# Kernel optimization log

Hardware: AMD Instinct MI355X
Metric: run time of the kernel (lower is better)

The kernel has to match this reference:

```python
import jax, jax.numpy as jnp
import numpy as np

H_IMG, W_IMG = 32, 32   # image_size -> seq_len = 1024
NH, HD, D = 8, 32, 256  # num_heads, head_dim, d_model
B = 8


def _relative_positions(h, w):
    # Swin-style relative position index table, [h*w, h*w] int32
    y = np.arange(h); x = np.arange(w)
    coords = np.stack(np.meshgrid(y, x, indexing='ij')).reshape(2, -1)  # [2, S]
    rel = coords[:, :, None] - coords[:, None, :]                      # [2, S, S]
    rel = rel.transpose(1, 2, 0).astype(np.int64)                      # [S, S, 2]
    rel[:, :, 0] += h - 1
    rel[:, :, 1] += w - 1
    rel[:, :, 0] *= 2 * w - 1
    return np.int32(rel.sum(-1))                                       # [S, S]

_POS = _relative_positions(H_IMG, W_IMG)


def setup_inputs() -> dict:
    key = jax.random.key(0)
    ks = jax.random.split(key, 8)
    S = H_IMG * W_IMG
    return {
        'inputs_q': jax.random.normal(ks[0], (B, S, D), jnp.float32),
        'inputs_kv': jax.random.normal(ks[1], (B, S, D), jnp.float32),
        'Wq': jax.random.normal(ks[2], (D, NH, HD), jnp.float32) / np.sqrt(D),
        'bq': jnp.zeros((NH, HD), jnp.float32),
        'Wk': jax.random.normal(ks[3], (D, NH, HD), jnp.float32) / np.sqrt(D),
        'bk': jnp.zeros((NH, HD), jnp.float32),
        'Wv': jax.random.normal(ks[4], (D, NH, HD), jnp.float32) / np.sqrt(D),
        'bv': jnp.zeros((NH, HD), jnp.float32),
        'rel_table': 0.02 * jax.random.normal(ks[5], ((2 * H_IMG - 1) * (2 * W_IMG - 1), NH), jnp.float32),
        'Wo': jax.random.normal(ks[6], (NH, HD, D), jnp.float32) / np.sqrt(NH * HD),
        'bo': jnp.zeros((D,), jnp.float32),
    }


def reference(inputs_q, inputs_kv, Wq, bq, Wk, bk, Wv, bv, rel_table, Wo, bo):
    pos = jnp.asarray(_POS)                                  # [S, S] int32 (constant)
    q = jnp.einsum('bsd,dhk->bshk', inputs_q, Wq) + bq       # [B, S, H, HD]
    k = jnp.einsum('bsd,dhk->bshk', inputs_kv, Wk) + bk
    v = jnp.einsum('bsd,dhk->bshk', inputs_kv, Wv) + bv
    q = q / jnp.sqrt(jnp.asarray(HD, q.dtype))
    attn = jnp.einsum('bqhd,bkhd->bhqk', q, k)               # [B, H, S, S]
    rel_bias = rel_table[pos]                                # [S, S, H]
    attn = attn + jnp.transpose(rel_bias, (2, 0, 1))[None]   # broadcast over batch
    attn = jax.nn.softmax(attn, axis=-1)
    x = jnp.einsum('bhqk,bkhd->bqhd', attn, v)               # [B, S, H, HD]
    return jnp.einsum('bqhd,hdf->bqf', x, Wo) + bo           # [B, S, D]
```

## Files before the change

kernel.cpp:

```cpp
#include <hip/hip_runtime.h>
#include <hip/hip_bf16.h>

#define B_SZ   8
#define S_LEN  1024
#define D_MOD  256
#define NHEADS 8
#define H_IMG  32
#define W_IMG  32
#define M_ROWS (B_SZ * S_LEN)
#define LOG2E  1.4426950408889634f
#define QSCALE_LOG2E 0.2550352766751165f

typedef _Float16 f16x8 __attribute__((ext_vector_type(8)));
typedef _Float16 f16x4 __attribute__((ext_vector_type(4)));
typedef float    f32x4 __attribute__((ext_vector_type(4)));

__global__ __launch_bounds__(256)
void wtrans_kernel(const float* __restrict__ Wq, const float* __restrict__ Wk,
                   const float* __restrict__ Wv, const float* __restrict__ Wo,
                   _Float16* __restrict__ wt) {
    const int mi = blockIdx.x >> 3;
    const int k0 = (blockIdx.x & 7) << 5;
    const float* W = (mi == 0) ? Wq : (mi == 1) ? Wk : (mi == 2) ? Wv : Wo;
    const int n = threadIdx.x;
    const float* src = W + (size_t)k0 * 256 + n;
    _Float16* dst = wt + (size_t)mi * 65536 + (size_t)n * 256 + k0;
#pragma unroll
    for (int g = 0; g < 4; ++g) {
        f16x8 o;
#pragma unroll
        for (int j = 0; j < 8; ++j) o[j] = (_Float16)src[(size_t)(g * 8 + j) * 256];
        *(f16x8*)(dst + g * 8) = o;
    }
}

__device__ inline void ldA16(const float* p, f16x8& x0, f16x8& x1) {
    f32x4 a = *(const f32x4*)p, b = *(const f32x4*)(p + 4);
    f32x4 c = *(const f32x4*)(p + 8), d = *(const f32x4*)(p + 12);
#pragma unroll
    for (int j = 0; j < 4; ++j) {
        x0[j] = (_Float16)a[j]; x0[4 + j] = (_Float16)b[j];
        x1[j] = (_Float16)c[j]; x1[4 + j] = (_Float16)d[j];
    }
}
__device__ inline void ldA16(const _Float16* p, f16x8& x0, f16x8& x1) {
    x0 = *(const f16x8*)p; x1 = *(const f16x8*)(p + 8);
}

template <typename InT, typename OutT, int VT_MODE>
__device__ inline void gemm_body(const InT* __restrict__ A, const _Float16* __restrict__ Wt,
                                 const float* __restrict__ bias, OutT* __restrict__ out,
                                 float scale, int m0, int n0) {
    __shared__ __align__(16) _Float16 As[2][64][72];
    __shared__ __align__(16) _Float16 Bt[2][64][72];
    const int tid  = threadIdx.x;
    const int w    = tid >> 6;
    const int lane = tid & 63;
    const int quad = lane >> 4;
    const int l16  = lane & 15;
    const int mq   = (w & 1) * 32;
    const int nq   = (w >> 1) * 32;

    const int srow = tid >> 2;
    const int scol = (tid & 3) << 4;
    const InT* Ap = A + (size_t)(m0 + srow) * 256 + scol;
    const _Float16* Bp = Wt + (size_t)(n0 + srow) * 256 + scol;

    f16x8 a0n, a1n, b0n, b1n;
    ldA16(Ap, a0n, a1n);
    b0n = *(const f16x8*)Bp; b1n = *(const f16x8*)(Bp + 8);
    *(f16x8*)(&As[0][srow][scol])     = a0n;
    *(f16x8*)(&As[0][srow][scol + 8]) = a1n;
    *(f16x8*)(&Bt[0][srow][scol])     = b0n;
    *(f16x8*)(&Bt[0][srow][scol + 8]) = b1n;
    __syncthreads();

    f32x4 acc[2][2];
#pragma unroll
    for (int i = 0; i < 2; ++i)
#pragma unroll
        for (int j = 0; j < 2; ++j) acc[i][j] = (f32x4){0.f, 0.f, 0.f, 0.f};

#pragma unroll
    for (int s = 0; s < 4; ++s) {
        const int cur = s & 1;
        if (s < 3) {
            ldA16(Ap + (s + 1) * 64, a0n, a1n);
            b0n = *(const f16x8*)(Bp + (s + 1) * 64);
            b1n = *(const f16x8*)(Bp + (s + 1) * 64 + 8);
        }
#pragma unroll
        for (int kk = 0; kk < 2; ++kk) {
            const int k8 = kk * 32 + quad * 8;
            f16x8 fa0 = *(const f16x8*)(&As[cur][mq + l16][k8]);
            f16x8 fa1 = *(const f16x8*)(&As[cur][mq + 16 + l16][k8]);
            f16x8 fb0 = *(const f16x8*)(&Bt[cur][nq + l16][k8]);
            f16x8 fb1 = *(const f16x8*)(&Bt[cur][nq + 16 + l16][k8]);
            acc[0][0] = __builtin_amdgcn_mfma_f32_16x16x32_f16(fa0, fb0, acc[0][0], 0, 0, 0);
            acc[0][1] = __builtin_amdgcn_mfma_f32_16x16x32_f16(fa0, fb1, acc[0][1], 0, 0, 0);
            acc[1][0] = __builtin_amdgcn_mfma_f32_16x16x32_f16(fa1, fb0, acc[1][0], 0, 0, 0);
            acc[1][1] = __builtin_amdgcn_mfma_f32_16x16x32_f16(fa1, fb1, acc[1][1], 0, 0, 0);
        }
        if (s < 3) {
            const int nxt = cur ^ 1;
            *(f16x8*)(&As[nxt][srow][scol])     = a0n;
            *(f16x8*)(&As[nxt][srow][scol + 8]) = a1n;
            *(f16x8*)(&Bt[nxt][srow][scol])     = b0n;
            *(f16x8*)(&Bt[nxt][srow][scol + 8]) = b1n;
            __syncthreads();
        }
    }

    if (VT_MODE) {
        const int b8 = (m0 >> 10) * 8;
#pragma unroll
        for (int nh = 0; nh < 2; ++nh) {
            const int col = n0 + nq + nh * 16 + l16;
            const float bv = bias[col];
#pragma unroll
            for (int mh = 0; mh < 2; ++mh) {
                const int row0 = (m0 & 1023) + mq + mh * 16 + quad * 4;
                f16x4 pk;
#pragma unroll
                for (int r = 0; r < 4; ++r) pk[r] = (_Float16)((acc[mh][nh][r] + bv) * scale);
                *(f16x4*)((_Float16*)out +
                          ((size_t)(b8 + (col >> 5)) * 32 + (col & 31)) * 1024 + row0) = pk;
            }
        }
    } else {
#pragma unroll
        for (int nh = 0; nh < 2; ++nh) {
            const int col = n0 + nq + nh * 16 + l16;
            const float bv = bias[col];
#pragma unroll
            for (int mh = 0; mh < 2; ++mh) {
#pragma unroll
                for (int r = 0; r < 4; ++r) {
                    const int row = m0 + mq + mh * 16 + quad * 4 + r;
                    out[(size_t)row * 256 + col] = (OutT)((acc[mh][nh][r] + bv) * scale);
                }
            }
        }
    }
}

__global__ __launch_bounds__(256)
void gemm_qkv_kernel(const float* __restrict__ in_q, const float* __restrict__ in_kv,
                     const _Float16* __restrict__ wt,
                     const float* __restrict__ bq, const float* __restrict__ bk,
                     const float* __restrict__ bv,
                     _Float16* __restrict__ qh, _Float16* __restrict__ kh,
                     _Float16* __restrict__ vt) {
    const int z = blockIdx.z;
    const int m0 = blockIdx.x * 64, n0 = blockIdx.y * 64;
    if (z == 0)
        gemm_body<float, _Float16, 0>(in_q, wt, bq, qh, QSCALE_LOG2E, m0, n0);
    else if (z == 1)
        gemm_body<float, _Float16, 0>(in_kv, wt + 65536, bk, kh, 1.0f, m0, n0);
    else
        gemm_body<float, _Float16, 1>(in_kv, wt + 2 * 65536, bv, vt, 1.0f, m0, n0);
}

__global__ __launch_bounds__(256)
void gemm_out_kernel(const _Float16* __restrict__ X, const _Float16* __restrict__ wt,
                     const float* __restrict__ bo, float* __restrict__ out) {
    gemm_body<_Float16, float, 0>(X, wt + (size_t)3 * 65536, bo, out, 1.0f,
                                  blockIdx.x * 64, blockIdx.y * 64);
}

__global__ __launch_bounds__(256)
void attn_kernel(const _Float16* __restrict__ q, const _Float16* __restrict__ k,
                 const _Float16* __restrict__ vt, const float* __restrict__ rel_table,
                 _Float16* __restrict__ xout) {
    __shared__ __align__(16) _Float16 Ps[4][2][32][40];
    __shared__ float bias_row[4][2][64];

    const int tid  = threadIdx.x;
    const int w    = tid >> 6;
    const int lane = tid & 63;
    const int quad = lane >> 4;
    const int l16  = lane & 15;

    const int n     = blockIdx.x;
    const int xcd   = n & 7;
    const int local = n >> 3;
    const int bh    = xcd * 8 + (local & 7);
    const int qc    = local >> 3;
    const int b     = bh >> 3, h = bh & 7;
    const int qrow_base = qc * 128 + w * 32;
    const int yq = qrow_base >> 5;

    const _Float16* qp = q + ((size_t)(b * S_LEN + qrow_base + l16)) * D_MOD + h * 32 + quad * 8;
    const f16x8 qf0 = *(const f16x8*)(qp);
    const f16x8 qf1 = *(const f16x8*)(qp + 16 * D_MOD);
    const _Float16* kp = k + ((size_t)(b * S_LEN + l16)) * D_MOD + h * 32 + quad * 8;
    const _Float16* vp = vt + ((size_t)(bh * 32 + l16)) * S_LEN + quad * 8;
    const float* bp = rel_table + ((size_t)(yq + 31) * 63 + lane) * NHEADS + h;

    f16x8 ones;
#pragma unroll
    for (int j = 0; j < 8; ++j) ones[j] = (_Float16)1.0f;

    f32x4 o00 = {0.f,0.f,0.f,0.f}, o01 = {0.f,0.f,0.f,0.f};
    f32x4 o10 = {0.f,0.f,0.f,0.f}, o11 = {0.f,0.f,0.f,0.f};
    f32x4 ol0 = {0.f,0.f,0.f,0.f}, ol1 = {0.f,0.f,0.f,0.f};

    if (lane < 63) bias_row[w][0][lane] = bp[0] * LOG2E;
    f16x8 kf0 = *(const f16x8*)(kp);
    f16x8 kf1 = *(const f16x8*)(kp + 16 * D_MOD);
    f16x8 vf0 = *(const f16x8*)(vp);
    f16x8 vf1 = *(const f16x8*)(vp + 16 * S_LEN);

    for (int kt = 0; kt < S_LEN / 32; ++kt) {
        const int cur = kt & 1, nxt = cur ^ 1;
        f16x8 nk0, nk1, nv0, nv1;
        float nb = 0.f;
        const bool more = (kt < S_LEN / 32 - 1);
        if (more) {
            const _Float16* kq = kp + (size_t)(kt + 1) * 32 * D_MOD;
            nk0 = *(const f16x8*)(kq);
            nk1 = *(const f16x8*)(kq + 16 * D_MOD);
            const _Float16* vq = vp + (kt + 1) * 32;
            nv0 = *(const f16x8*)(vq);
            nv1 = *(const f16x8*)(vq + 16 * S_LEN);
            if (lane < 63) nb = bp[-(ptrdiff_t)((kt + 1) * 63 * NHEADS)];
        }

#pragma unroll
        for (int mh = 0; mh < 2; ++mh) {
            const f16x8 qf = mh ? qf1 : qf0;
#pragma unroll
            for (int kh = 0; kh < 2; ++kh) {
                const int idx0 = mh * 16 + quad * 4 - kh * 16 - l16 + 31;
                const float* bb = &bias_row[w][cur][idx0];
                f32x4 c; c[0] = bb[0]; c[1] = bb[1]; c[2] = bb[2]; c[3] = bb[3];
                f32x4 s = __builtin_amdgcn_mfma_f32_16x16x32_f16(qf, kh ? kf1 : kf0, c, 0, 0, 0);
#pragma unroll
                for (int r = 0; r < 4; ++r)
                    Ps[w][cur][mh * 16 + quad * 4 + r][kh * 16 + l16] =
                        (_Float16)__builtin_amdgcn_exp2f(s[r]);
            }
        }

        const f16x8 pf0 = *(const f16x8*)(&Ps[w][cur][l16][quad * 8]);
        const f16x8 pf1 = *(const f16x8*)(&Ps[w][cur][16 + l16][quad * 8]);
        o00 = __builtin_amdgcn_mfma_f32_16x16x32_f16(pf0, vf0, o00, 0, 0, 0);
        o01 = __builtin_amdgcn_mfma_f32_16x16x32_f16(pf0, vf1, o01, 0, 0, 0);
        o10 = __builtin_amdgcn_mfma_f32_16x16x32_f16(pf1, vf0, o10, 0, 0, 0);
        o11 = __builtin_amdgcn_mfma_f32_16x16x32_f16(pf1, vf1, o11, 0, 0, 0);
        ol0 = __builtin_amdgcn_mfma_f32_16x16x32_f16(pf0, ones, ol0, 0, 0, 0);
        ol1 = __builtin_amdgcn_mfma_f32_16x16x32_f16(pf1, ones, ol1, 0, 0, 0);

        if (more) {
            if (lane < 63) bias_row[w][nxt][lane] = nb * LOG2E;
            kf0 = nk0; kf1 = nk1; vf0 = nv0; vf1 = nv1;
        }
    }

#pragma unroll
    for (int mh = 0; mh < 2; ++mh) {
        const f32x4 oa = mh ? o10 : o00;
        const f32x4 ob = mh ? o11 : o01;
        const f32x4 ll = mh ? ol1 : ol0;
#pragma unroll
        for (int r = 0; r < 4; ++r) {
            const float inv = __builtin_amdgcn_rcpf(ll[r]);
            const int qg = qrow_base + mh * 16 + quad * 4 + r;
            _Float16* op = xout + ((size_t)(b * S_LEN + qg)) * D_MOD + h * 32;
            op[l16]      = (_Float16)(oa[r] * inv);
            op[l16 + 16] = (_Float16)(ob[r] * inv);
        }
    }
}

extern "C" void kernel_launch(void* const* d_in, const int* in_sizes, int n_in,
                              void* d_out, int out_size, void* d_ws, size_t ws_size,
                              hipStream_t stream) {
    const float* in_q  = (const float*)d_in[0];
    const float* in_kv = (const float*)d_in[1];
    const float* Wq    = (const float*)d_in[2];
    const float* bq    = (const float*)d_in[3];
    const float* Wk    = (const float*)d_in[4];
    const float* bk    = (const float*)d_in[5];
    const float* Wv    = (const float*)d_in[6];
    const float* bv    = (const float*)d_in[7];
    const float* rel   = (const float*)d_in[8];
    const float* Wo    = (const float*)d_in[9];
    const float* bo    = (const float*)d_in[10];
    float* out = (float*)d_out;

    _Float16* qh = (_Float16*)d_ws;
    _Float16* kh = qh + (size_t)M_ROWS * D_MOD;
    _Float16* vt = kh + (size_t)M_ROWS * D_MOD;
    _Float16* xh = vt + (size_t)M_ROWS * D_MOD;
    _Float16* wt = xh + (size_t)M_ROWS * D_MOD;

    const dim3 blk(256);

    wtrans_kernel<<<dim3(32), blk, 0, stream>>>(Wq, Wk, Wv, Wo, wt);
    gemm_qkv_kernel<<<dim3(M_ROWS / 64, 4, 3), blk, 0, stream>>>(
        in_q, in_kv, wt, bq, bk, bv, qh, kh, vt);
    attn_kernel<<<dim3(512), blk, 0, stream>>>(qh, kh, vt, rel, xh);
    gemm_out_kernel<<<dim3(M_ROWS / 64, 4), blk, 0, stream>>>(xh, wt, bo, out);
}
```

Baseline: 142.9 us.

## Split attention keys across blocks, precompute bias table, fuse combine into output GEMM

Attention now splits the key range into two halves across twice as many blocks. Each block writes unnormalized fp32 partial outputs and row sums, and the output GEMM merges and normalizes them while loading its A operand. The relative-position bias is precomputed once into an MFMA-layout table in a merged prep kernel, which replaces the per-tile LDS staging, and the MFMA operands are swapped so P is written to LDS as vectorized stores. The GEMMs drop LDS double buffering for single buffers with an extra barrier and gain occupancy hints. The aim is more parallelism in attention and fewer LDS/bias ops, at the cost of extra fp32 partial traffic.

```diff
diff --git a/kernel.cpp b/kernel.cpp
--- a/kernel.cpp
+++ b/kernel.cpp
@@ -1,39 +1,19 @@
 #include <hip/hip_runtime.h>
-#include <hip/hip_bf16.h>
 
 #define B_SZ   8
 #define S_LEN  1024
 #define D_MOD  256
 #define NHEADS 8
-#define H_IMG  32
-#define W_IMG  32
 #define M_ROWS (B_SZ * S_LEN)
 #define LOG2E  1.4426950408889634f
 #define QSCALE_LOG2E 0.2550352766751165f
+#define NSPLIT 2
+#define TILES_PER_SPLIT 16
 
 typedef _Float16 f16x8 __attribute__((ext_vector_type(8)));
 typedef _Float16 f16x4 __attribute__((ext_vector_type(4)));
 typedef float    f32x4 __attribute__((ext_vector_type(4)));
 
-__global__ __launch_bounds__(256)
-void wtrans_kernel(const float* __restrict__ Wq, const float* __restrict__ Wk,
-                   const float* __restrict__ Wv, const float* __restrict__ Wo,
-                   _Float16* __restrict__ wt) {
-    const int mi = blockIdx.x >> 3;
-    const int k0 = (blockIdx.x & 7) << 5;
-    const float* W = (mi == 0) ? Wq : (mi == 1) ? Wk : (mi == 2) ? Wv : Wo;
-    const int n = threadIdx.x;
-    const float* src = W + (size_t)k0 * 256 + n;
-    _Float16* dst = wt + (size_t)mi * 65536 + (size_t)n * 256 + k0;
-#pragma unroll
-    for (int g = 0; g < 4; ++g) {
-        f16x8 o;
-#pragma unroll
-        for (int j = 0; j < 8; ++j) o[j] = (_Float16)src[(size_t)(g * 8 + j) * 256];
-        *(f16x8*)(dst + g * 8) = o;
-    }
-}
-
 __device__ inline void ldA16(const float* p, f16x8& x0, f16x8& x1) {
     f32x4 a = *(const f32x4*)p, b = *(const f32x4*)(p + 4);
     f32x4 c = *(const f32x4*)(p + 8), d = *(const f32x4*)(p + 12);
@@ -45,14 +25,52 @@
 }
 __device__ inline void ldA16(const _Float16* p, f16x8& x0, f16x8& x1) {
     x0 = *(const f16x8*)p; x1 = *(const f16x8*)(p + 8);
+}
+
+__global__ __launch_bounds__(256)
+void prep_kernel(const float* __restrict__ Wq, const float* __restrict__ Wk,
+                 const float* __restrict__ Wv, const float* __restrict__ Wo,
+                 const float* __restrict__ rel,
+                 _Float16* __restrict__ wt, float* __restrict__ tab) {
+    if (blockIdx.x < 32) {
+        const int mi = blockIdx.x >> 3;
+        const int k0 = (blockIdx.x & 7) << 5;
+        const float* W = (mi == 0) ? Wq : (mi == 1) ? Wk : (mi == 2) ? Wv : Wo;
+        const int n = threadIdx.x;
+        const float* src = W + (size_t)k0 * 256 + n;
+        _Float16* dst = wt + (size_t)mi * 65536 + (size_t)n * 256 + k0;
+#pragma unroll
+        for (int g = 0; g < 4; ++g) {
+            f16x8 o;
+#pragma unroll
+            for (int j = 0; j < 8; ++j) o[j] = (_Float16)src[(size_t)(g * 8 + j) * 256];
+            *(f16x8*)(dst + g * 8) = o;
+        }
+        return;
+    }
+    const int flat = (blockIdx.x - 32) * 256 + threadIdx.x;
+    const int lane = flat & 63;
+    const int t1   = flat >> 6;
+    const int e    = t1 % 3;
+    const int t2   = t1 / 3;
+    const int dy31 = t2 % 63;
+    const int h    = t2 / 63;
+    const int quad = lane >> 4, l16 = lane & 15;
+    f32x4 v;
+#pragma unroll
+    for (int reg = 0; reg < 4; ++reg) {
+        const int idx = 16 * e + l16 - quad * 4 - reg + 15;
+        v[reg] = rel[(size_t)(dy31 * 63 + idx) * NHEADS + h] * LOG2E;
+    }
+    *(f32x4*)(tab + (size_t)flat * 4) = v;
 }
 
 template <typename InT, typename OutT, int VT_MODE>
 __device__ inline void gemm_body(const InT* __restrict__ A, const _Float16* __restrict__ Wt,
                                  const float* __restrict__ bias, OutT* __restrict__ out,
                                  float scale, int m0, int n0) {
-    __shared__ __align__(16) _Float16 As[2][64][72];
-    __shared__ __align__(16) _Float16 Bt[2][64][72];
+    __shared__ __align__(16) _Float16 As[64][72];
+    __shared__ __align__(16) _Float16 Bt[64][72];
     const int tid  = threadIdx.x;
     const int w    = tid >> 6;
     const int lane = tid & 63;
@@ -69,11 +87,6 @@
     f16x8 a0n, a1n, b0n, b1n;
     ldA16(Ap, a0n, a1n);
     b0n = *(const f16x8*)Bp; b1n = *(const f16x8*)(Bp + 8);
-    *(f16x8*)(&As[0][srow][scol])     = a0n;
-    *(f16x8*)(&As[0][srow][scol + 8]) = a1n;
-    *(f16x8*)(&Bt[0][srow][scol])     = b0n;
-    *(f16x8*)(&Bt[0][srow][scol + 8]) = b1n;
-    __syncthreads();
 
     f32x4 acc[2][2];
 #pragma unroll
@@ -83,7 +96,12 @@
 
 #pragma unroll
     for (int s = 0; s < 4; ++s) {
-        const int cur = s & 1;
+        if (s) __syncthreads();
+        *(f16x8*)(&As[srow][scol])     = a0n;
+        *(f16x8*)(&As[srow][scol + 8]) = a1n;
+        *(f16x8*)(&Bt[srow][scol])     = b0n;
+        *(f16x8*)(&Bt[srow][scol + 8]) = b1n;
+        __syncthreads();
         if (s < 3) {
             ldA16(Ap + (s + 1) * 64, a0n, a1n);
             b0n = *(const f16x8*)(Bp + (s + 1) * 64);
@@ -92,22 +110,14 @@
 #pragma unroll
         for (int kk = 0; kk < 2; ++kk) {
             const int k8 = kk * 32 + quad * 8;
-            f16x8 fa0 = *(const f16x8*)(&As[cur][mq + l16][k8]);
-            f16x8 fa1 = *(const f16x8*)(&As[cur][mq + 16 + l16][k8]);
-            f16x8 fb0 = *(const f16x8*)(&Bt[cur][nq + l16][k8]);
-            f16x8 fb1 = *(const f16x8*)(&Bt[cur][nq + 16 + l16][k8]);
+            f16x8 fa0 = *(const f16x8*)(&As[mq + l16][k8]);
+            f16x8 fa1 = *(const f16x8*)(&As[mq + 16 + l16][k8]);
+            f16x8 fb0 = *(const f16x8*)(&Bt[nq + l16][k8]);
+            f16x8 fb1 = *(const f16x8*)(&Bt[nq + 16 + l16][k8]);
             acc[0][0] = __builtin_amdgcn_mfma_f32_16x16x32_f16(fa0, fb0, acc[0][0], 0, 0, 0);
             acc[0][1] = __builtin_amdgcn_mfma_f32_16x16x32_f16(fa0, fb1, acc[0][1], 0, 0, 0);
             acc[1][0] = __builtin_amdgcn_mfma_f32_16x16x32_f16(fa1, fb0, acc[1][0], 0, 0, 0);
             acc[1][1] = __builtin_amdgcn_mfma_f32_16x16x32_f16(fa1, fb1, acc[1][1], 0, 0, 0);
-        }
-        if (s < 3) {
-            const int nxt = cur ^ 1;
-            *(f16x8*)(&As[nxt][srow][scol])     = a0n;
-            *(f16x8*)(&As[nxt][srow][scol + 8]) = a1n;
-            *(f16x8*)(&Bt[nxt][srow][scol])     = b0n;
-            *(f16x8*)(&Bt[nxt][srow][scol + 8]) = b1n;
-            __syncthreads();
         }
     }
 
@@ -144,7 +154,7 @@
     }
 }
 
-__global__ __launch_bounds__(256)
+__global__ __launch_bounds__(256, 6)
 void gemm_qkv_kernel(const float* __restrict__ in_q, const float* __restrict__ in_kv,
                      const _Float16* __restrict__ wt,
                      const float* __restrict__ bq, const float* __restrict__ bk,
@@ -162,40 +172,127 @@
 }
 
 __global__ __launch_bounds__(256)
-void gemm_out_kernel(const _Float16* __restrict__ X, const _Float16* __restrict__ wt,
-                     const float* __restrict__ bo, float* __restrict__ out) {
-    gemm_body<_Float16, float, 0>(X, wt + (size_t)3 * 65536, bo, out, 1.0f,
-                                  blockIdx.x * 64, blockIdx.y * 64);
-}
-
-__global__ __launch_bounds__(256)
-void attn_kernel(const _Float16* __restrict__ q, const _Float16* __restrict__ k,
-                 const _Float16* __restrict__ vt, const float* __restrict__ rel_table,
-                 _Float16* __restrict__ xout) {
-    __shared__ __align__(16) _Float16 Ps[4][2][32][40];
-    __shared__ float bias_row[4][2][64];
-
+void gemm_out_kernel(const float* __restrict__ o0, const float* __restrict__ o1,
+                     const float* __restrict__ l0, const float* __restrict__ l1,
+                     const _Float16* __restrict__ wt4, const float* __restrict__ bo,
+                     float* __restrict__ out) {
+    __shared__ __align__(16) _Float16 As[64][72];
+    __shared__ __align__(16) _Float16 Bt[64][72];
     const int tid  = threadIdx.x;
     const int w    = tid >> 6;
     const int lane = tid & 63;
     const int quad = lane >> 4;
     const int l16  = lane & 15;
+    const int mq   = (w & 1) * 32;
+    const int nq   = (w >> 1) * 32;
+    const int m0   = blockIdx.x * 64, n0 = blockIdx.y * 64;
+
+    const int srow = tid >> 2;
+    const int scol = (tid & 3) << 4;
+    const size_t row = (size_t)(m0 + srow);
+    const _Float16* Bp = wt4 + (size_t)(n0 + srow) * 256 + scol;
+
+    f16x8 a0n, a1n, b0n, b1n;
+    auto ldX = [&](int s, f16x8& x0, f16x8& x1) {
+        const int col0 = s * 64 + scol;
+        const int head = col0 >> 5;
+        const float inv = __builtin_amdgcn_rcpf(l0[row * 8 + head] + l1[row * 8 + head]);
+        const float* p0 = o0 + row * 256 + col0;
+        const float* p1 = o1 + row * 256 + col0;
+        f32x4 u0 = *(const f32x4*)p0,       u1 = *(const f32x4*)(p0 + 4);
+        f32x4 u2 = *(const f32x4*)(p0 + 8), u3 = *(const f32x4*)(p0 + 12);
+        f32x4 v0 = *(const f32x4*)p1,       v1 = *(const f32x4*)(p1 + 4);
+        f32x4 v2 = *(const f32x4*)(p1 + 8), v3 = *(const f32x4*)(p1 + 12);
+#pragma unroll
+        for (int j = 0; j < 4; ++j) {
+            x0[j]     = (_Float16)((u0[j] + v0[j]) * inv);
+            x0[4 + j] = (_Float16)((u1[j] + v1[j]) * inv);
+            x1[j]     = (_Float16)((u2[j] + v2[j]) * inv);
+            x1[4 + j] = (_Float16)((u3[j] + v3[j]) * inv);
+        }
+    };
+
+    ldX(0, a0n, a1n);
+    b0n = *(const f16x8*)Bp; b1n = *(const f16x8*)(Bp + 8);
+
+    f32x4 acc[2][2];
+#pragma unroll
+    for (int i = 0; i < 2; ++i)
+#pragma unroll
+        for (int j = 0; j < 2; ++j) acc[i][j] = (f32x4){0.f, 0.f, 0.f, 0.f};
+
+#pragma unroll
+    for (int s = 0; s < 4; ++s) {
+        if (s) __syncthreads();
+        *(f16x8*)(&As[srow][scol])     = a0n;
+        *(f16x8*)(&As[srow][scol + 8]) = a1n;
+        *(f16x8*)(&Bt[srow][scol])     = b0n;
+        *(f16x8*)(&Bt[srow][scol + 8]) = b1n;
+        __syncthreads();
+        if (s < 3) {
+            ldX(s + 1, a0n, a1n);
+            b0n = *(const f16x8*)(Bp + (s + 1) * 64);
+            b1n = *(const f16x8*)(Bp + (s + 1) * 64 + 8);
+        }
+#pragma unroll
+        for (int kk = 0; kk < 2; ++kk) {
+            const int k8 = kk * 32 + quad * 8;
+            f16x8 fa0 = *(const f16x8*)(&As[mq + l16][k8]);
+            f16x8 fa1 = *(const f16x8*)(&As[mq + 16 + l16][k8]);
+            f16x8 fb0 = *(const f16x8*)(&Bt[nq + l16][k8]);
+            f16x8 fb1 = *(const f16x8*)(&Bt[nq + 16 + l16][k8]);
+            acc[0][0] = __builtin_amdgcn_mfma_f32_16x16x32_f16(fa0, fb0, acc[0][0], 0, 0, 0);
+            acc[0][1] = __builtin_amdgcn_mfma_f32_16x16x32_f16(fa0, fb1, acc[0][1], 0, 0, 0);
+            acc[1][0] = __builtin_amdgcn_mfma_f32_16x16x32_f16(fa1, fb0, acc[1][0], 0, 0, 0);
+            acc[1][1] = __builtin_amdgcn_mfma_f32_16x16x32_f16(fa1, fb1, acc[1][1], 0, 0, 0);
+        }
+    }
+
+#pragma unroll
+    for (int nh = 0; nh < 2; ++nh) {
+        const int col = n0 + nq + nh * 16 + l16;
+        const float bv = bo[col];
+#pragma unroll
+        for (int mh = 0; mh < 2; ++mh) {
+#pragma unroll
+            for (int r = 0; r < 4; ++r) {
+                const int rr = m0 + mq + mh * 16 + quad * 4 + r;
+                out[(size_t)rr * 256 + col] = (acc[mh][nh][r] + bv);
+            }
+        }
+    }
+}
+
+__global__ __launch_bounds__(256, 4)
+void attn_kernel(const _Float16* __restrict__ q, const _Float16* __restrict__ k,
+                 const _Float16* __restrict__ vt, const float* __restrict__ tab,
+                 float* __restrict__ opart, float* __restrict__ lpart) {
+    __shared__ __align__(16) _Float16 Ps[4][32][40];
+
+    const int tid  = threadIdx.x;
+    const int w    = tid >> 6;
+    const int lane = tid & 63;
+    const int quad = lane >> 4;
+    const int l16  = lane & 15;
 
     const int n     = blockIdx.x;
     const int xcd   = n & 7;
     const int local = n >> 3;
     const int bh    = xcd * 8 + (local & 7);
-    const int qc    = local >> 3;
-    const int b     = bh >> 3, h = bh & 7;
+    const int rest  = local >> 3;
+    const int qc    = rest & 7;
+    const int split = rest >> 3;
+    const int b = bh >> 3, h = bh & 7;
     const int qrow_base = qc * 128 + w * 32;
     const int yq = qrow_base >> 5;
+    const int key0 = split * (TILES_PER_SPLIT * 32);
 
     const _Float16* qp = q + ((size_t)(b * S_LEN + qrow_base + l16)) * D_MOD + h * 32 + quad * 8;
     const f16x8 qf0 = *(const f16x8*)(qp);
     const f16x8 qf1 = *(const f16x8*)(qp + 16 * D_MOD);
-    const _Float16* kp = k + ((size_t)(b * S_LEN + l16)) * D_MOD + h * 32 + quad * 8;
-    const _Float16* vp = vt + ((size_t)(bh * 32 + l16)) * S_LEN + quad * 8;
-    const float* bp = rel_table + ((size_t)(yq + 31) * 63 + lane) * NHEADS + h;
+    const _Float16* kp = k + ((size_t)(b * S_LEN + key0 + l16)) * D_MOD + h * 32 + quad * 8;
+    const _Float16* vp = vt + ((size_t)(bh * 32 + l16)) * S_LEN + key0 + quad * 8;
+    const float* tabh = tab + (size_t)h * 63 * 3 * 256;
 
     f16x8 ones;
 #pragma unroll
@@ -205,71 +302,70 @@
     f32x4 o10 = {0.f,0.f,0.f,0.f}, o11 = {0.f,0.f,0.f,0.f};
     f32x4 ol0 = {0.f,0.f,0.f,0.f}, ol1 = {0.f,0.f,0.f,0.f};
 
-    if (lane < 63) bias_row[w][0][lane] = bp[0] * LOG2E;
     f16x8 kf0 = *(const f16x8*)(kp);
     f16x8 kf1 = *(const f16x8*)(kp + 16 * D_MOD);
     f16x8 vf0 = *(const f16x8*)(vp);
     f16x8 vf1 = *(const f16x8*)(vp + 16 * S_LEN);
 
-    for (int kt = 0; kt < S_LEN / 32; ++kt) {
-        const int cur = kt & 1, nxt = cur ^ 1;
+    for (int t = 0; t < TILES_PER_SPLIT; ++t) {
         f16x8 nk0, nk1, nv0, nv1;
-        float nb = 0.f;
-        const bool more = (kt < S_LEN / 32 - 1);
+        const bool more = (t < TILES_PER_SPLIT - 1);
         if (more) {
-            const _Float16* kq = kp + (size_t)(kt + 1) * 32 * D_MOD;
+            const _Float16* kq = kp + (size_t)(t + 1) * 32 * D_MOD;
             nk0 = *(const f16x8*)(kq);
             nk1 = *(const f16x8*)(kq + 16 * D_MOD);
-            const _Float16* vq = vp + (kt + 1) * 32;
+            const _Float16* vq = vp + (t + 1) * 32;
             nv0 = *(const f16x8*)(vq);
             nv1 = *(const f16x8*)(vq + 16 * S_LEN);
-            if (lane < 63) nb = bp[-(ptrdiff_t)((kt + 1) * 63 * NHEADS)];
-        }
-
-#pragma unroll
-        for (int mh = 0; mh < 2; ++mh) {
-            const f16x8 qf = mh ? qf1 : qf0;
-#pragma unroll
-            for (int kh = 0; kh < 2; ++kh) {
-                const int idx0 = mh * 16 + quad * 4 - kh * 16 - l16 + 31;
-                const float* bb = &bias_row[w][cur][idx0];
-                f32x4 c; c[0] = bb[0]; c[1] = bb[1]; c[2] = bb[2]; c[3] = bb[3];
-                f32x4 s = __builtin_amdgcn_mfma_f32_16x16x32_f16(qf, kh ? kf1 : kf0, c, 0, 0, 0);
-#pragma unroll
-                for (int r = 0; r < 4; ++r)
-                    Ps[w][cur][mh * 16 + quad * 4 + r][kh * 16 + l16] =
-                        (_Float16)__builtin_amdgcn_exp2f(s[r]);
-            }
-        }
-
-        const f16x8 pf0 = *(const f16x8*)(&Ps[w][cur][l16][quad * 8]);
-        const f16x8 pf1 = *(const f16x8*)(&Ps[w][cur][16 + l16][quad * 8]);
-        o00 = __builtin_amdgcn_mfma_f32_16x16x32_f16(pf0, vf0, o00, 0, 0, 0);
-        o01 = __builtin_amdgcn_mfma_f32_16x16x32_f16(pf0, vf1, o01, 0, 0, 0);
-        o10 = __builtin_amdgcn_mfma_f32_16x16x32_f16(pf1, vf0, o10, 0, 0, 0);
-        o11 = __builtin_amdgcn_mfma_f32_16x16x32_f16(pf1, vf1, o11, 0, 0, 0);
-        ol0 = __builtin_amdgcn_mfma_f32_16x16x32_f16(pf0, ones, ol0, 0, 0, 0);
-        ol1 = __builtin_amdgcn_mfma_f32_16x16x32_f16(pf1, ones, ol1, 0, 0, 0);
-
-        if (more) {
-            if (lane < 63) bias_row[w][nxt][lane] = nb * LOG2E;
-            kf0 = nk0; kf1 = nk1; vf0 = nv0; vf1 = nv1;
-        }
-    }
-
+        }
+
+        const int dy31 = yq + 31 - (split * TILES_PER_SPLIT + t);
+        const float* tb = tabh + (size_t)dy31 * 3 * 256 + lane * 4;
+        const f32x4 c0 = *(const f32x4*)(tb);
+        const f32x4 c1 = *(const f32x4*)(tb + 256);
+        const f32x4 c2 = *(const f32x4*)(tb + 512);
+
+        f32x4 s00 = __builtin_amdgcn_mfma_f32_16x16x32_f16(kf0, qf0, c1, 0, 0, 0);
+        f32x4 s01 = __builtin_amdgcn_mfma_f32_16x16x32_f16(kf1, qf0, c0, 0, 0, 0);
+        f32x4 s10 = __builtin_amdgcn_mfma_f32_16x16x32_f16(kf0, qf1, c2, 0, 0, 0);
+        f32x4 s11 = __builtin_amdgcn_mfma_f32_16x16x32_f16(kf1, qf1, c1, 0, 0, 0);
+
+        f16x4 p;
+#pragma unroll
+        for (int r = 0; r < 4; ++r) p[r] = (_Float16)__builtin_amdgcn_exp2f(s00[r]);
+        *(f16x4*)(&Ps[w][l16][quad * 4]) = p;
+#pragma unroll
+        for (int r = 0; r < 4; ++r) p[r] = (_Float16)__builtin_amdgcn_exp2f(s01[r]);
+        *(f16x4*)(&Ps[w][l16][16 + quad * 4]) = p;
+#pragma unroll
+        for (int r = 0; r < 4; ++r) p[r] = (_Float16)__builtin_amdgcn_exp2f(s10[r]);
+        *(f16x4*)(&Ps[w][16 + l16][quad * 4]) = p;
+#pragma unroll
+        for (int r = 0; r < 4; ++r) p[r] = (_Float16)__builtin_amdgcn_exp2f(s11[r]);
+        *(f16x4*)(&Ps[w][16 + l16][16 + quad * 4]) = p;
+
+        const f16x8 pf0 = *(const f16x8*)(&Ps[w][l16][quad * 8]);
+        const f16x8 pf1 = *(const f16x8*)(&Ps[w][16 + l16][quad * 8]);
+        o00 = __builtin_amdgcn_mfma_f32_16x16x32_f16(vf0, pf0, o00, 0, 0, 0);
+        o01 = __builtin_amdgcn_mfma_f32_16x16x32_f16(vf1, pf0, o01, 0, 0, 0);
+        o10 = __builtin_amdgcn_mfma_f32_16x16x32_f16(vf0, pf1, o10, 0, 0, 0);
+        o11 = __builtin_amdgcn_mfma_f32_16x16x32_f16(vf1, pf1, o11, 0, 0, 0);
+        ol0 = __builtin_amdgcn_mfma_f32_16x16x32_f16(ones, pf0, ol0, 0, 0, 0);
+        ol1 = __builtin_amdgcn_mfma_f32_16x16x32_f16(ones, pf1, ol1, 0, 0, 0);
+
+        if (more) { kf0 = nk0; kf1 = nk1; vf0 = nv0; vf1 = nv1; }
+    }
+
+    float* ob = opart + (size_t)split * M_ROWS * D_MOD;
+    float* lb = lpart + (size_t)split * M_ROWS * NHEADS;
 #pragma unroll
     for (int mh = 0; mh < 2; ++mh) {
-        const f32x4 oa = mh ? o10 : o00;
-        const f32x4 ob = mh ? o11 : o01;
-        const f32x4 ll = mh ? ol1 : ol0;
-#pragma unroll
-        for (int r = 0; r < 4; ++r) {
-            const float inv = __builtin_amdgcn_rcpf(ll[r]);
-            const int qg = qrow_base + mh * 16 + quad * 4 + r;
-            _Float16* op = xout + ((size_t)(b * S_LEN + qg)) * D_MOD + h * 32;
-            op[l16]      = (_Float16)(oa[r] * inv);
-            op[l16 + 16] = (_Float16)(ob[r] * inv);
-        }
+        const int qg = qrow_base + 16 * mh + l16;
+        float* op = ob + ((size_t)(b * S_LEN + qg)) * D_MOD + h * 32 + quad * 4;
+        *(f32x4*)(op)      = mh ? o10 : o00;
+        *(f32x4*)(op + 16) = mh ? o11 : o01;
+        if (quad == 0)
+            lb[(size_t)(b * S_LEN + qg) * NHEADS + h] = mh ? ol1[0] : ol0[0];
     }
 }
 
@@ -289,17 +385,23 @@
     const float* bo    = (const float*)d_in[10];
     float* out = (float*)d_out;
 
-    _Float16* qh = (_Float16*)d_ws;
-    _Float16* kh = qh + (size_t)M_ROWS * D_MOD;
-    _Float16* vt = kh + (size_t)M_ROWS * D_MOD;
-    _Float16* xh = vt + (size_t)M_ROWS * D_MOD;
-    _Float16* wt = xh + (size_t)M_ROWS * D_MOD;
+    char* wsb = (char*)d_ws;
+    _Float16* qh    = (_Float16*)(wsb);
+    _Float16* kh    = (_Float16*)(wsb + (size_t)4  * 1048576);
+    _Float16* vt    = (_Float16*)(wsb + (size_t)8  * 1048576);
+    float*    opart = (float*)  (wsb + (size_t)12 * 1048576);
+    float*    lpart = (float*)  (wsb + (size_t)28 * 1048576);
+    _Float16* wt    = (_Float16*)(wsb + (size_t)29 * 1048576);
+    float*    tab   = (float*)  (wsb + (size_t)30 * 1048576);
 
     const dim3 blk(256);
 
-    wtrans_kernel<<<dim3(32), blk, 0, stream>>>(Wq, Wk, Wv, Wo, wt);
+    prep_kernel<<<dim3(410), blk, 0, stream>>>(Wq, Wk, Wv, Wo, rel, wt, tab);
     gemm_qkv_kernel<<<dim3(M_ROWS / 64, 4, 3), blk, 0, stream>>>(
         in_q, in_kv, wt, bq, bk, bv, qh, kh, vt);
-    attn_kernel<<<dim3(512), blk, 0, stream>>>(qh, kh, vt, rel, xh);
-    gemm_out_kernel<<<dim3(M_ROWS / 64, 4), blk, 0, stream>>>(xh, wt, bo, out);
-}
+    attn_kernel<<<dim3(1024), blk, 0, stream>>>(qh, kh, vt, tab, opart, lpart);
+    gemm_out_kernel<<<dim3(M_ROWS / 64, 4), blk, 0, stream>>>(
+        opart, opart + (size_t)M_ROWS * D_MOD,
+        lpart, lpart + (size_t)M_ROWS * NHEADS,
+        wt + (size_t)3 * 65536, bo, out);
+}
```

Result: no change. 142.7 us (-0.1%).
